# Optimization experiments

Measured on AMD Instinct MI355X. Metric: run time of the kernel, lower is better.

The kernel has to match this reference:

```python
import jax, jax.numpy as jnp
import numpy as np

IN_DIMS = 512
TOKEN_DIM = 512
NUM_HEADS = 1
D = TOKEN_DIM * NUM_HEADS
SCALE = TOKEN_DIM ** (-0.5)
EPS = 1e-12  # torch F.normalize default


def _l2norm(v, axis):
    n = jnp.sqrt(jnp.sum(v * v, axis=axis, keepdims=True))
    return v / jnp.maximum(n, EPS)


def setup_inputs() -> dict:
    key = jax.random.key(0)
    ks = jax.random.split(key, 10)
    B, C, H, W = 64, IN_DIMS, 28, 28
    s_in = IN_DIMS ** -0.5
    s_d = D ** -0.5
    return {
        "x": jax.random.normal(ks[0], (B, C, H, W), jnp.float32),
        "Wq": jax.random.normal(ks[1], (IN_DIMS, D), jnp.float32) * s_in,
        "bq": jax.random.normal(ks[2], (D,), jnp.float32) * 0.01,
        "Wk": jax.random.normal(ks[3], (IN_DIMS, D), jnp.float32) * s_in,
        "bk": jax.random.normal(ks[4], (D,), jnp.float32) * 0.01,
        "w_g": jax.random.normal(ks[5], (D, 1), jnp.float32),
        "Wp": jax.random.normal(ks[6], (D, D), jnp.float32) * s_d,
        "bp": jax.random.normal(ks[7], (D,), jnp.float32) * 0.01,
        "Wf": jax.random.normal(ks[8], (D, TOKEN_DIM), jnp.float32) * s_d,
        "bf": jax.random.normal(ks[9], (TOKEN_DIM,), jnp.float32) * 0.01,
    }


def reference(x, Wq, bq, Wk, bk, w_g, Wp, bp, Wf, bf):
    B, C, H, W = x.shape
    t = x.reshape(B, C, H * W).transpose(0, 2, 1)          # [B, N, C]
    query = _l2norm(t @ Wq + bq, axis=-1)                  # [B, N, D]
    k = _l2norm(t @ Wk + bk, axis=-1)                      # [B, N, D]
    attn = _l2norm((query @ w_g) * SCALE, axis=1)          # [B, N, 1], normalized over tokens
    ctx = jnp.sum(attn * query, axis=1, keepdims=True)     # [B, 1, D] global context
    out = (ctx * k) @ Wp + bp + query                      # [B, N, D]
    out = out @ Wf + bf                                    # [B, N, TOKEN_DIM]
    return out.transpose(0, 2, 1).reshape(B, -1, H, W)
```

## Files before the change

### kernel.cpp

```cpp
#include <hip/hip_runtime.h>

#define EPSN 1e-12f
#define SCALE_F 0.044194173824159216f

typedef __bf16 bf16x8 __attribute__((ext_vector_type(8)));
typedef __bf16 bf16x4 __attribute__((ext_vector_type(4)));
typedef float  f32x4  __attribute__((ext_vector_type(4)));

__device__ __forceinline__ void gld16(const void* src, void* dst) {
  __builtin_amdgcn_global_load_lds(
      (const __attribute__((address_space(1))) unsigned int*)src,
      (__attribute__((address_space(3))) unsigned int*)dst, 16, 0, 0);
}

#define BARRIER_W4() do { \
  asm volatile("s_waitcnt vmcnt(4) lgkmcnt(0)" ::: "memory"); \
  __builtin_amdgcn_sched_barrier(0); \
  __builtin_amdgcn_s_barrier(); \
  __builtin_amdgcn_sched_barrier(0); } while (0)

__global__ __launch_bounds__(256) void k_prep_t(const float* __restrict__ Wq,
                                                const float* __restrict__ Wk,
                                                __bf16* __restrict__ WqT,
                                                __bf16* __restrict__ WkT) {
  __shared__ float Tq[32][33], Tk[32][33];
  const int c0 = blockIdx.x * 32, d0 = blockIdx.y * 32;
  const int dx = threadIdx.x, cy = threadIdx.y;
  #pragma unroll
  for (int p = 0; p < 4; ++p) {
    int c = cy + p * 8;
    Tq[c][dx] = Wq[(size_t)(c0 + c) * 512 + d0 + dx];
    Tk[c][dx] = Wk[(size_t)(c0 + c) * 512 + d0 + dx];
  }
  __syncthreads();
  #pragma unroll
  for (int p = 0; p < 4; ++p) {
    int d = cy + p * 8;
    WqT[(size_t)(d0 + d) * 512 + c0 + dx] = (__bf16)Tq[dx][d];
    WkT[(size_t)(d0 + d) * 512 + c0 + dx] = (__bf16)Tk[dx][d];
  }
}

__global__ __launch_bounds__(512) void k_prep_w(const float* __restrict__ Wp,
                                                const float* __restrict__ Wf,
                                                const float* __restrict__ bp,
                                                const float* __restrict__ bfv,
                                                __bf16* __restrict__ WcT,
                                                float* __restrict__ bpf) {
  int kk = blockIdx.x;
  int d  = threadIdx.x;
  float a0 = 0.f, a1 = 0.f, a2 = 0.f, a3 = 0.f;
  for (int c = 0; c < 512; c += 4) {
    a0 = fmaf(Wp[kk * 512 + c],     Wf[(size_t)c * 512 + d],         a0);
    a1 = fmaf(Wp[kk * 512 + c + 1], Wf[(size_t)(c + 1) * 512 + d],   a1);
    a2 = fmaf(Wp[kk * 512 + c + 2], Wf[(size_t)(c + 2) * 512 + d],   a2);
    a3 = fmaf(Wp[kk * 512 + c + 3], Wf[(size_t)(c + 3) * 512 + d],   a3);
  }
  WcT[(size_t)d * 1024 + kk]       = (__bf16)((a0 + a1) + (a2 + a3));
  WcT[(size_t)d * 1024 + 512 + kk] = (__bf16)Wf[(size_t)kk * 512 + d];
  if (kk == 0) {
    float b0 = 0.f, b1 = 0.f;
    for (int c = 0; c < 512; c += 2) {
      b0 = fmaf(bp[c],     Wf[(size_t)c * 512 + d],       b0);
      b1 = fmaf(bp[c + 1], Wf[(size_t)(c + 1) * 512 + d], b1);
    }
    bpf[d] = b0 + b1 + bfv[d];
  }
}

__global__ __launch_bounds__(512, 4) void k_qk(const float* __restrict__ x,
                                               const __bf16* __restrict__ WqT,
                                               const __bf16* __restrict__ WkT,
                                               const float* __restrict__ bq,
                                               const float* __restrict__ bk,
                                               const float* __restrict__ wg,
                                               __bf16* __restrict__ Qn,
                                               __bf16* __restrict__ Kn,
                                               float* __restrict__ pctx,
                                               float* __restrict__ pgsq) {
  __shared__ __align__(1024) unsigned char stg[2][36864];
  __shared__ float red[8][64], redG[8][64], invv[64], gs[64];
  const int t = threadIdx.x, lane = t & 63, w = t >> 6;
  const int li = lane & 15, lq = lane >> 4;
  const int isK = blockIdx.x & 1, nx = blockIdx.x >> 1;
  const int n0 = nx * 64, b = blockIdx.y;
  const __bf16* Wt  = isK ? WkT : WqT;
  const float* bias = isK ? bk : bq;
  __bf16* dst       = isK ? Kn : Qn;

  const int ra = w & 3, h = w >> 2;
  const int tok = ra * 16 + li;
  int nc = n0 + tok; if (nc > 783) nc = 783;
  const float* xbase = x + ((size_t)b * 512 + lq * 8 + h * 4) * 784 + nc;
  const __bf16* wsrc = Wt + (size_t)li * 512 + lq * 8;

  float xA[4], xB[4];
  f32x4 acc[4][4] = {};

  auto loadX = [&](float (&xr)[4], int ks) {
    if (ks > 15) ks = 15;
    #pragma unroll
    for (int j = 0; j < 4; ++j)
      xr[j] = xbase[(size_t)(ks * 32 + j) * 784];
  };
  auto stageB = [&](int buf, int ks) {
    #pragma unroll
    for (int i = 0; i < 4; ++i) {
      int r = w * 4 + i;
      gld16(wsrc + (size_t)r * 16 * 512 + ks * 32, stg[buf] + 4096 + r * 1024);
    }
  };
  auto writeA = [&](int buf, const float (&xr)[4]) {
    bf16x4 v;
    #pragma unroll
    for (int j = 0; j < 4; ++j) v[j] = (__bf16)xr[j];
    *(bf16x4*)(stg[buf] + ra * 1024 + lane * 16 + h * 8) = v;
  };
  auto mstep = [&](int buf) {
    bf16x8 af[4];
    #pragma unroll
    for (int rb = 0; rb < 4; ++rb)
      af[rb] = *(const bf16x8*)(stg[buf] + rb * 1024 + lane * 16);
    #pragma unroll
    for (int cb = 0; cb < 4; ++cb) {
      bf16x8 bf = *(const bf16x8*)(stg[buf] + 4096 + (w * 4 + cb) * 1024 + lane * 16);
      #pragma unroll
      for (int rb = 0; rb < 4; ++rb)
        acc[rb][cb] = __builtin_amdgcn_mfma_f32_16x16x32_bf16(af[rb], bf, acc[rb][cb], 0, 0, 0);
    }
  };

  loadX(xA, 0); loadX(xB, 1);
  stageB(0, 0); writeA(0, xA);
  __builtin_amdgcn_sched_barrier(0);
  loadX(xA, 2);
  BARRIER_W4();

  #pragma unroll 1
  for (int k = 0; k < 16; k += 2) {
    stageB(1, k + 1); writeA(1, xB);
    __builtin_amdgcn_sched_barrier(0);
    loadX(xB, k + 3);
    mstep(0);
    BARRIER_W4();
    if (k + 2 < 16) { stageB(0, k + 2); writeA(0, xA); }
    __builtin_amdgcn_sched_barrier(0);
    loadX(xA, k + 4);
    mstep(1);
    BARRIER_W4();
  }

  float bv[4], wv[4];
  #pragma unroll
  for (int cb = 0; cb < 4; ++cb) {
    int col = w * 64 + cb * 16 + li;
    bv[cb] = bias[col];
    wv[cb] = isK ? 0.f : wg[col];
  }
  #pragma unroll
  for (int rb = 0; rb < 4; ++rb)
    #pragma unroll
    for (int cb = 0; cb < 4; ++cb)
      #pragma unroll
      for (int j = 0; j < 4; ++j)
        acc[rb][cb][j] += bv[cb];
  #pragma unroll
  for (int rb = 0; rb < 4; ++rb)
    #pragma unroll
    for (int j = 0; j < 4; ++j) {
      float ss = 0.f, sg = 0.f;
      #pragma unroll
      for (int cb = 0; cb < 4; ++cb) {
        float v = acc[rb][cb][j];
        ss = fmaf(v, v, ss); sg = fmaf(v, wv[cb], sg);
      }
      ss += __shfl_xor(ss, 1); ss += __shfl_xor(ss, 2); ss += __shfl_xor(ss, 4); ss += __shfl_xor(ss, 8);
      sg += __shfl_xor(sg, 1); sg += __shfl_xor(sg, 2); sg += __shfl_xor(sg, 4); sg += __shfl_xor(sg, 8);
      if (li == 0) {
        int row = rb * 16 + lq * 4 + j;
        red[w][row] = ss; redG[w][row] = sg;
      }
    }
  __syncthreads();
  if (t < 64) {
    float ss = 0.f, sg = 0.f;
    #pragma unroll
    for (int wv2 = 0; wv2 < 8; ++wv2) { ss += red[wv2][t]; sg += redG[wv2][t]; }
    float iv = 1.f / fmaxf(sqrtf(ss), EPSN);
    invv[t] = iv;
    if (!isK) {
      float gv = (n0 + t < 784) ? sg * iv : 0.f;
      gs[t] = gv;
      float pg = gv * gv;
      pg += __shfl_xor(pg, 1);  pg += __shfl_xor(pg, 2);  pg += __shfl_xor(pg, 4);
      pg += __shfl_xor(pg, 8);  pg += __shfl_xor(pg, 16); pg += __shfl_xor(pg, 32);
      if (t == 0) pgsq[b * 13 + nx] = pg;
    }
  }
  __syncthreads();
  float pc[4] = {0.f, 0.f, 0.f, 0.f};
  #pragma unroll
  for (int rb = 0; rb < 4; ++rb)
    #pragma unroll
    for (int j = 0; j < 4; ++j) {
      int row = rb * 16 + lq * 4 + j;
      if (n0 + row < 784) {
        float iv = invv[row];
        float gr = isK ? 0.f : gs[row];
        size_t base = ((size_t)b * 784 + n0 + row) * 512 + w * 64 + li;
        #pragma unroll
        for (int cb = 0; cb < 4; ++cb) {
          float qv = acc[rb][cb][j] * iv;
          dst[base + cb * 16] = (__bf16)qv;
          pc[cb] = fmaf(gr, qv, pc[cb]);
        }
      }
    }
  if (!isK) {
    #pragma unroll
    for (int cb = 0; cb < 4; ++cb) {
      pc[cb] += __shfl_xor(pc[cb], 16);
      pc[cb] += __shfl_xor(pc[cb], 32);
    }
    if (lq == 0) {
      #pragma unroll
      for (int cb = 0; cb < 4; ++cb)
        pctx[((size_t)b * 13 + nx) * 512 + w * 64 + cb * 16 + li] = pc[cb];
    }
  }
}

__global__ __launch_bounds__(512) void k_ctx2(const float* __restrict__ pctx,
                                              const float* __restrict__ pgsq,
                                              float* __restrict__ ctx) {
  const int b = blockIdx.x, t = threadIdx.x;
  float tot = 0.f;
  #pragma unroll
  for (int i = 0; i < 13; ++i) tot += pgsq[b * 13 + i];
  float alpha = SCALE_F / fmaxf(sqrtf(tot) * SCALE_F, EPSN);
  float s = 0.f;
  #pragma unroll
  for (int i = 0; i < 13; ++i) s += pctx[((size_t)b * 13 + i) * 512 + t];
  ctx[(size_t)b * 512 + t] = alpha * s;
}

__global__ __launch_bounds__(512) void k_kc(__bf16* __restrict__ Kn,
                                            const float* __restrict__ ctx) {
  const int b = blockIdx.y;
  const int chunk = blockIdx.x * 512 + threadIdx.x;
  const int row = chunk >> 6;
  const int c8 = (chunk & 63) * 8;
  __bf16* p = Kn + ((size_t)b * 784 + row) * 512 + c8;
  const float* cp = ctx + b * 512 + c8;
  bf16x8 v = *(const bf16x8*)p;
  #pragma unroll
  for (int j = 0; j < 8; ++j) v[j] = (__bf16)((float)v[j] * cp[j]);
  *(bf16x8*)p = v;
}

__global__ __launch_bounds__(512, 4) void k_out(const __bf16* __restrict__ Qn,
                                                const __bf16* __restrict__ Kc,
                                                const __bf16* __restrict__ WcT,
                                                const float* __restrict__ bpf,
                                                float* __restrict__ out) {
  __shared__ __align__(1024) unsigned char stg[2][36864];
  const int t = threadIdx.x, lane = t & 63, w = t >> 6;
  const int li = lane & 15, lq = lane >> 4;
  const int n0 = blockIdx.x * 64, b = blockIdx.y;
  f32x4 acc[4][4] = {};

  auto stage = [&](int buf, int ks) {
    const __bf16* Ap = (ks < 16) ? Kc : Qn;
    const int kA = (ks & 15) * 32;
    #pragma unroll
    for (int i = 0; i < 5; ++i) {
      int r = w + i * 8;
      if (r < 36) {
        if (r < 4) {
          int row = n0 + r * 16 + li; if (row > 783) row = 783;
          gld16(Ap + ((size_t)b * 784 + row) * 512 + kA + lq * 8, stg[buf] + r * 1024);
        } else {
          gld16(WcT + (size_t)((r - 4) * 16 + li) * 1024 + ks * 32 + lq * 8,
                stg[buf] + 4096 + (r - 4) * 1024);
        }
      }
    }
  };
  auto mstep = [&](const unsigned char* s) {
    bf16x8 af[4];
    #pragma unroll
    for (int rb = 0; rb < 4; ++rb)
      af[rb] = *(const bf16x8*)(s + rb * 1024 + lane * 16);
    #pragma unroll
    for (int cb = 0; cb < 4; ++cb) {
      bf16x8 bf = *(const bf16x8*)(s + 4096 + (w * 4 + cb) * 1024 + lane * 16);
      #pragma unroll
      for (int rb = 0; rb < 4; ++rb)
        acc[rb][cb] = __builtin_amdgcn_mfma_f32_16x16x32_bf16(af[rb], bf, acc[rb][cb], 0, 0, 0);
    }
  };

  stage(0, 0);
  __syncthreads();
  #pragma unroll 1
  for (int ks = 0; ks < 32; ++ks) {
    if (ks + 1 < 32) stage((ks + 1) & 1, ks + 1);
    mstep(stg[ks & 1]);
    __syncthreads();
  }

  float bv[4];
  #pragma unroll
  for (int cb = 0; cb < 4; ++cb) bv[cb] = bpf[w * 64 + cb * 16 + li];
  #pragma unroll
  for (int rb = 0; rb < 4; ++rb) {
    int nrow = n0 + rb * 16 + lq * 4;
    if (nrow < 784) {
      #pragma unroll
      for (int cb = 0; cb < 4; ++cb) {
        f32x4 v;
        #pragma unroll
        for (int j = 0; j < 4; ++j) v[j] = acc[rb][cb][j] + bv[cb];
        *(f32x4*)&out[((size_t)b * 512 + w * 64 + cb * 16 + li) * 784 + nrow] = v;
      }
    }
  }
}

extern "C" void kernel_launch(void* const* d_in, const int* in_sizes, int n_in,
                              void* d_out, int out_size, void* d_ws, size_t ws_size,
                              hipStream_t stream) {
  const float* x   = (const float*)d_in[0];
  const float* Wq  = (const float*)d_in[1];
  const float* bq  = (const float*)d_in[2];
  const float* Wk  = (const float*)d_in[3];
  const float* bk  = (const float*)d_in[4];
  const float* wg  = (const float*)d_in[5];
  const float* Wp  = (const float*)d_in[6];
  const float* bp  = (const float*)d_in[7];
  const float* Wf  = (const float*)d_in[8];
  const float* bfv = (const float*)d_in[9];
  float* out = (float*)d_out;
  char* ws = (char*)d_ws;

  const size_t SZQN = (size_t)64 * 784 * 512 * 2;
  __bf16* Qn   = (__bf16*)(ws);
  __bf16* Kn   = (__bf16*)(ws + SZQN);
  __bf16* WqT  = (__bf16*)(ws + 2 * SZQN);
  __bf16* WkT  = (__bf16*)(ws + 2 * SZQN + 524288);
  __bf16* WcT  = (__bf16*)(ws + 2 * SZQN + 2 * 524288);
  float*  bpf  = (float*) (ws + 2 * SZQN + 2 * 524288 + 1048576);
  float*  pctx = (float*) (ws + 2 * SZQN + 2 * 524288 + 1048576 + 2048);
  float*  pgsq = (float*) (ws + 2 * SZQN + 2 * 524288 + 1048576 + 2048 + 1703936);
  float*  ctx  = (float*) (ws + 2 * SZQN + 2 * 524288 + 1048576 + 2048 + 1703936 + 4096);

  k_prep_t<<<dim3(16, 16), dim3(32, 8), 0, stream>>>(Wq, Wk, WqT, WkT);
  k_prep_w<<<dim3(512),    dim3(512),   0, stream>>>(Wp, Wf, bp, bfv, WcT, bpf);
  k_qk    <<<dim3(26, 64), dim3(512),   0, stream>>>(x, WqT, WkT, bq, bk, wg, Qn, Kn, pctx, pgsq);
  k_ctx2  <<<dim3(64),     dim3(512),   0, stream>>>(pctx, pgsq, ctx);
  k_kc    <<<dim3(98, 64), dim3(512),   0, stream>>>(Kn, ctx);
  k_out   <<<dim3(13, 64), dim3(512),   0, stream>>>(Qn, Kn, WcT, bpf, out);
}
```

Before: 386.2 us.

## Triple-buffer QK and output GEMMs, fuse ctx scaling into output A-tile staging

Converts the QK projection kernel from a double-buffered loop to a fully unrolled triple-buffered pipeline with explicit vmcnt waits. Removes the separate k_kc pass that scaled Kn by ctx in place. The output GEMM now loads K/Q rows through registers, multiplies by ctx from LDS before writing the A tile, and splits output columns across two 256-thread blocks with its own triple-buffered pipeline. This saves a full read-modify-write over Kn and one launch, and aims to hide load latency better. In exchange it uses more LDS per block and adds redundant A loads across the column split.

Result: slower. 448.0 us (+16.0%).

```diff
diff --git a/kernel.cpp b/kernel.cpp
--- a/kernel.cpp
+++ b/kernel.cpp
@@ -12,12 +12,6 @@
       (const __attribute__((address_space(1))) unsigned int*)src,
       (__attribute__((address_space(3))) unsigned int*)dst, 16, 0, 0);
 }
-
-#define BARRIER_W4() do { \
-  asm volatile("s_waitcnt vmcnt(4) lgkmcnt(0)" ::: "memory"); \
-  __builtin_amdgcn_sched_barrier(0); \
-  __builtin_amdgcn_s_barrier(); \
-  __builtin_amdgcn_sched_barrier(0); } while (0)
 
 __global__ __launch_bounds__(256) void k_prep_t(const float* __restrict__ Wq,
                                                 const float* __restrict__ Wk,
@@ -68,17 +62,17 @@
   }
 }
 
-__global__ __launch_bounds__(512, 4) void k_qk(const float* __restrict__ x,
-                                               const __bf16* __restrict__ WqT,
-                                               const __bf16* __restrict__ WkT,
-                                               const float* __restrict__ bq,
-                                               const float* __restrict__ bk,
-                                               const float* __restrict__ wg,
-                                               __bf16* __restrict__ Qn,
-                                               __bf16* __restrict__ Kn,
-                                               float* __restrict__ pctx,
-                                               float* __restrict__ pgsq) {
-  __shared__ __align__(1024) unsigned char stg[2][36864];
+__global__ __launch_bounds__(512) void k_qk(const float* __restrict__ x,
+                                            const __bf16* __restrict__ WqT,
+                                            const __bf16* __restrict__ WkT,
+                                            const float* __restrict__ bq,
+                                            const float* __restrict__ bk,
+                                            const float* __restrict__ wg,
+                                            __bf16* __restrict__ Qn,
+                                            __bf16* __restrict__ Kn,
+                                            float* __restrict__ pctx,
+                                            float* __restrict__ pgsq) {
+  __shared__ __align__(1024) unsigned char stg[3][36864];
   __shared__ float red[8][64], redG[8][64], invv[64], gs[64];
   const int t = threadIdx.x, lane = t & 63, w = t >> 6;
   const int li = lane & 15, lq = lane >> 4;
@@ -89,8 +83,7 @@
   __bf16* dst       = isK ? Kn : Qn;
 
   const int ra = w & 3, h = w >> 2;
-  const int tok = ra * 16 + li;
-  int nc = n0 + tok; if (nc > 783) nc = 783;
+  int nc = n0 + ra * 16 + li; if (nc > 783) nc = 783;
   const float* xbase = x + ((size_t)b * 512 + lq * 8 + h * 4) * 784 + nc;
   const __bf16* wsrc = Wt + (size_t)li * 512 + lq * 8;
 
@@ -98,16 +91,17 @@
   f32x4 acc[4][4] = {};
 
   auto loadX = [&](float (&xr)[4], int ks) {
-    if (ks > 15) ks = 15;
+    int kk = ks > 15 ? 15 : ks;
     #pragma unroll
     for (int j = 0; j < 4; ++j)
-      xr[j] = xbase[(size_t)(ks * 32 + j) * 784];
+      xr[j] = xbase[(size_t)(kk * 32 + j) * 784];
   };
   auto stageB = [&](int buf, int ks) {
+    int kk = ks > 15 ? 15 : ks;
     #pragma unroll
     for (int i = 0; i < 4; ++i) {
       int r = w * 4 + i;
-      gld16(wsrc + (size_t)r * 16 * 512 + ks * 32, stg[buf] + 4096 + r * 1024);
+      gld16(wsrc + (size_t)r * 16 * 512 + kk * 32, stg[buf] + 4096 + r * 1024);
     }
   };
   auto writeA = [&](int buf, const float (&xr)[4]) {
@@ -131,24 +125,33 @@
   };
 
   loadX(xA, 0); loadX(xB, 1);
-  stageB(0, 0); writeA(0, xA);
-  __builtin_amdgcn_sched_barrier(0);
+  stageB(0, 0); stageB(1, 1);
+  asm volatile("s_waitcnt vmcnt(12)" ::: "memory");
+  __builtin_amdgcn_sched_barrier(0);
+  writeA(0, xA);
   loadX(xA, 2);
-  BARRIER_W4();
-
-  #pragma unroll 1
-  for (int k = 0; k < 16; k += 2) {
-    stageB(1, k + 1); writeA(1, xB);
-    __builtin_amdgcn_sched_barrier(0);
-    loadX(xB, k + 3);
-    mstep(0);
-    BARRIER_W4();
-    if (k + 2 < 16) { stageB(0, k + 2); writeA(0, xA); }
-    __builtin_amdgcn_sched_barrier(0);
-    loadX(xA, k + 4);
-    mstep(1);
-    BARRIER_W4();
-  }
+  asm volatile("s_waitcnt vmcnt(8) lgkmcnt(0)" ::: "memory");
+  __builtin_amdgcn_sched_barrier(0);
+  writeA(1, xB);
+  __builtin_amdgcn_sched_barrier(0);
+  __builtin_amdgcn_s_barrier();
+
+#define QK_STEP(S, XNEW, XWR) \
+  loadX(XNEW, (S) + 3); \
+  stageB(((S) + 2) % 3, (S) + 2); \
+  mstep((S) % 3); \
+  asm volatile("s_waitcnt vmcnt(8) lgkmcnt(0)" ::: "memory"); \
+  __builtin_amdgcn_sched_barrier(0); \
+  writeA(((S) + 2) % 3, XWR); \
+  __builtin_amdgcn_sched_barrier(0); \
+  __builtin_amdgcn_s_barrier();
+
+  QK_STEP(0,  xB, xA)  QK_STEP(1,  xA, xB)  QK_STEP(2,  xB, xA)  QK_STEP(3,  xA, xB)
+  QK_STEP(4,  xB, xA)  QK_STEP(5,  xA, xB)  QK_STEP(6,  xB, xA)  QK_STEP(7,  xA, xB)
+  QK_STEP(8,  xB, xA)  QK_STEP(9,  xA, xB)  QK_STEP(10, xB, xA)  QK_STEP(11, xA, xB)
+  QK_STEP(12, xB, xA)  QK_STEP(13, xA, xB)  QK_STEP(14, xB, xA)  QK_STEP(15, xA, xB)
+#undef QK_STEP
+  asm volatile("s_waitcnt vmcnt(0)" ::: "memory");
 
   float bv[4], wv[4];
   #pragma unroll
@@ -244,74 +247,111 @@
   ctx[(size_t)b * 512 + t] = alpha * s;
 }
 
-__global__ __launch_bounds__(512) void k_kc(__bf16* __restrict__ Kn,
-                                            const float* __restrict__ ctx) {
-  const int b = blockIdx.y;
-  const int chunk = blockIdx.x * 512 + threadIdx.x;
-  const int row = chunk >> 6;
-  const int c8 = (chunk & 63) * 8;
-  __bf16* p = Kn + ((size_t)b * 784 + row) * 512 + c8;
-  const float* cp = ctx + b * 512 + c8;
-  bf16x8 v = *(const bf16x8*)p;
-  #pragma unroll
-  for (int j = 0; j < 8; ++j) v[j] = (__bf16)((float)v[j] * cp[j]);
-  *(bf16x8*)p = v;
-}
-
-__global__ __launch_bounds__(512, 4) void k_out(const __bf16* __restrict__ Qn,
-                                                const __bf16* __restrict__ Kc,
+__global__ __launch_bounds__(256, 2) void k_out(const __bf16* __restrict__ Qn,
+                                                const __bf16* __restrict__ Kn,
+                                                const float* __restrict__ ctx,
                                                 const __bf16* __restrict__ WcT,
                                                 const float* __restrict__ bpf,
                                                 float* __restrict__ out) {
-  __shared__ __align__(1024) unsigned char stg[2][36864];
+  __shared__ __align__(1024) unsigned char stg[3][20480];
+  __shared__ float ctx_lds[1024];
   const int t = threadIdx.x, lane = t & 63, w = t >> 6;
   const int li = lane & 15, lq = lane >> 4;
-  const int n0 = blockIdx.x * 64, b = blockIdx.y;
+  const int n0 = blockIdx.x * 64, d0 = blockIdx.y * 256, b = blockIdx.z;
+
+  #pragma unroll
+  for (int i = 0; i < 4; ++i) {
+    int idx = t + i * 256;
+    ctx_lds[idx] = (idx < 512) ? ctx[(size_t)b * 512 + idx] : 1.0f;
+  }
+  __syncthreads();
+
+  const int rg = t >> 6, ch = t & 63;
+  const int kq8 = (ch >> 4) * 8;
+  int rowg = n0 + rg * 16 + (ch & 15); if (rowg > 783) rowg = 783;
+  const size_t rowbase = ((size_t)b * 784 + rowg) * 512;
+  const __bf16* wsrc = WcT + (size_t)(d0 + li) * 1024 + lq * 8;
+
+  bf16x8 aA, aB;
   f32x4 acc[4][4] = {};
 
-  auto stage = [&](int buf, int ks) {
-    const __bf16* Ap = (ks < 16) ? Kc : Qn;
-    const int kA = (ks & 15) * 32;
-    #pragma unroll
-    for (int i = 0; i < 5; ++i) {
-      int r = w + i * 8;
-      if (r < 36) {
-        if (r < 4) {
-          int row = n0 + r * 16 + li; if (row > 783) row = 783;
-          gld16(Ap + ((size_t)b * 784 + row) * 512 + kA + lq * 8, stg[buf] + r * 1024);
-        } else {
-          gld16(WcT + (size_t)((r - 4) * 16 + li) * 1024 + ks * 32 + lq * 8,
-                stg[buf] + 4096 + (r - 4) * 1024);
-        }
-      }
-    }
-  };
-  auto mstep = [&](const unsigned char* s) {
+  auto loadA = [&](bf16x8& ar, int ks) {
+    int kk = ks > 31 ? 31 : ks;
+    int kl = kk * 32 + kq8;
+    const __bf16* src = (kl < 512) ? (Kn + rowbase + kl) : (Qn + rowbase + kl - 512);
+    ar = *(const bf16x8*)src;
+  };
+  auto stageB = [&](int buf, int ks) {
+    int kk = ks > 31 ? 31 : ks;
+    #pragma unroll
+    for (int i = 0; i < 4; ++i) {
+      int r = w * 4 + i;
+      gld16(wsrc + (size_t)r * 16 * 1024 + kk * 32, stg[buf] + 4096 + r * 1024);
+    }
+  };
+  auto writeA = [&](int buf, bf16x8 ar, int ks) {
+    int kk = ks > 31 ? 31 : ks;
+    int kl = kk * 32 + kq8;
+    f32x4 c0 = *(const f32x4*)&ctx_lds[kl];
+    f32x4 c1 = *(const f32x4*)&ctx_lds[kl + 4];
+    bf16x8 r;
+    #pragma unroll
+    for (int j = 0; j < 4; ++j) {
+      r[j]     = (__bf16)((float)ar[j]     * c0[j]);
+      r[4 + j] = (__bf16)((float)ar[4 + j] * c1[j]);
+    }
+    *(bf16x8*)(stg[buf] + rg * 1024 + ch * 16) = r;
+  };
+  auto mstep = [&](int buf) {
     bf16x8 af[4];
     #pragma unroll
     for (int rb = 0; rb < 4; ++rb)
-      af[rb] = *(const bf16x8*)(s + rb * 1024 + lane * 16);
+      af[rb] = *(const bf16x8*)(stg[buf] + rb * 1024 + lane * 16);
     #pragma unroll
     for (int cb = 0; cb < 4; ++cb) {
-      bf16x8 bf = *(const bf16x8*)(s + 4096 + (w * 4 + cb) * 1024 + lane * 16);
+      bf16x8 bf = *(const bf16x8*)(stg[buf] + 4096 + (w * 4 + cb) * 1024 + lane * 16);
       #pragma unroll
       for (int rb = 0; rb < 4; ++rb)
         acc[rb][cb] = __builtin_amdgcn_mfma_f32_16x16x32_bf16(af[rb], bf, acc[rb][cb], 0, 0, 0);
     }
   };
 
-  stage(0, 0);
-  __syncthreads();
-  #pragma unroll 1
-  for (int ks = 0; ks < 32; ++ks) {
-    if (ks + 1 < 32) stage((ks + 1) & 1, ks + 1);
-    mstep(stg[ks & 1]);
-    __syncthreads();
-  }
+  loadA(aA, 0); loadA(aB, 1);
+  stageB(0, 0); stageB(1, 1);
+  asm volatile("s_waitcnt vmcnt(9)" ::: "memory");
+  __builtin_amdgcn_sched_barrier(0);
+  writeA(0, aA, 0);
+  loadA(aA, 2);
+  asm volatile("s_waitcnt vmcnt(5) lgkmcnt(0)" ::: "memory");
+  __builtin_amdgcn_sched_barrier(0);
+  writeA(1, aB, 1);
+  __builtin_amdgcn_sched_barrier(0);
+  __builtin_amdgcn_s_barrier();
+
+#define OUT_STEP(S, ANEW, AWR) \
+  loadA(ANEW, (S) + 3); \
+  stageB(((S) + 2) % 3, (S) + 2); \
+  mstep((S) % 3); \
+  asm volatile("s_waitcnt vmcnt(5) lgkmcnt(0)" ::: "memory"); \
+  __builtin_amdgcn_sched_barrier(0); \
+  writeA(((S) + 2) % 3, AWR, (S) + 2); \
+  __builtin_amdgcn_sched_barrier(0); \
+  __builtin_amdgcn_s_barrier();
+
+  OUT_STEP(0,  aB, aA)  OUT_STEP(1,  aA, aB)  OUT_STEP(2,  aB, aA)  OUT_STEP(3,  aA, aB)
+  OUT_STEP(4,  aB, aA)  OUT_STEP(5,  aA, aB)  OUT_STEP(6,  aB, aA)  OUT_STEP(7,  aA, aB)
+  OUT_STEP(8,  aB, aA)  OUT_STEP(9,  aA, aB)  OUT_STEP(10, aB, aA)  OUT_STEP(11, aA, aB)
+  OUT_STEP(12, aB, aA)  OUT_STEP(13, aA, aB)  OUT_STEP(14, aB, aA)  OUT_STEP(15, aA, aB)
+  OUT_STEP(16, aB, aA)  OUT_STEP(17, aA, aB)  OUT_STEP(18, aB, aA)  OUT_STEP(19, aA, aB)
+  OUT_STEP(20, aB, aA)  OUT_STEP(21, aA, aB)  OUT_STEP(22, aB, aA)  OUT_STEP(23, aA, aB)
+  OUT_STEP(24, aB, aA)  OUT_STEP(25, aA, aB)  OUT_STEP(26, aB, aA)  OUT_STEP(27, aA, aB)
+  OUT_STEP(28, aB, aA)  OUT_STEP(29, aA, aB)  OUT_STEP(30, aB, aA)  OUT_STEP(31, aA, aB)
+#undef OUT_STEP
+  asm volatile("s_waitcnt vmcnt(0)" ::: "memory");
 
   float bv[4];
   #pragma unroll
-  for (int cb = 0; cb < 4; ++cb) bv[cb] = bpf[w * 64 + cb * 16 + li];
+  for (int cb = 0; cb < 4; ++cb) bv[cb] = bpf[d0 + w * 64 + cb * 16 + li];
   #pragma unroll
   for (int rb = 0; rb < 4; ++rb) {
     int nrow = n0 + rb * 16 + lq * 4;
@@ -321,7 +361,7 @@
         f32x4 v;
         #pragma unroll
         for (int j = 0; j < 4; ++j) v[j] = acc[rb][cb][j] + bv[cb];
-        *(f32x4*)&out[((size_t)b * 512 + w * 64 + cb * 16 + li) * 784 + nrow] = v;
+        *(f32x4*)&out[((size_t)b * 512 + d0 + w * 64 + cb * 16 + li) * 784 + nrow] = v;
       }
     }
   }
@@ -354,10 +394,9 @@
   float*  pgsq = (float*) (ws + 2 * SZQN + 2 * 524288 + 1048576 + 2048 + 1703936);
   float*  ctx  = (float*) (ws + 2 * SZQN + 2 * 524288 + 1048576 + 2048 + 1703936 + 4096);
 
-  k_prep_t<<<dim3(16, 16), dim3(32, 8), 0, stream>>>(Wq, Wk, WqT, WkT);
-  k_prep_w<<<dim3(512),    dim3(512),   0, stream>>>(Wp, Wf, bp, bfv, WcT, bpf);
-  k_qk    <<<dim3(26, 64), dim3(512),   0, stream>>>(x, WqT, WkT, bq, bk, wg, Qn, Kn, pctx, pgsq);
-  k_ctx2  <<<dim3(64),     dim3(512),   0, stream>>>(pctx, pgsq, ctx);
-  k_kc    <<<dim3(98, 64), dim3(512),   0, stream>>>(Kn, ctx);
-  k_out   <<<dim3(13, 64), dim3(512),   0, stream>>>(Qn, Kn, WcT, bpf, out);
-}
+  k_prep_t<<<dim3(16, 16),    dim3(32, 8), 0, stream>>>(Wq, Wk, WqT, WkT);
+  k_prep_w<<<dim3(512),       dim3(512),   0, stream>>>(Wp, Wf, bp, bfv, WcT, bpf);
+  k_qk    <<<dim3(26, 64),    dim3(512),   0, stream>>>(x, WqT, WkT, bq, bk, wg, Qn, Kn, pctx, pgsq);
+  k_ctx2  <<<dim3(64),        dim3(512),   0, stream>>>(pctx, pgsq, ctx);
+  k_out   <<<dim3(13, 2, 64), dim3(256),   0, stream>>>(Qn, Kn, ctx, WcT, bpf, out);
+}
```
